# Optimization experiments

Measured on AMD Instinct MI355X. Metric: run time of the kernel, lower is better.

Reference implementation:

```python
import jax, jax.numpy as jnp
import numpy as np

B, C, H, W = 4, 64, 128, 128
K = 9  # 3x3 kernel taps
OFFSET_SCALE = 1.0
EPS = 1e-5


def conv2d(x, w, b):
    # x: [B,Cin,H,W], w: [Cout,Cin,3,3] -> [B,Cout,H,W] (SAME padding, stride 1)
    out = jax.lax.conv_general_dilated(x, w, (1, 1), 'SAME',
                                       dimension_numbers=('NCHW', 'OIHW', 'NCHW'))
    return out + b[None, :, None, None]


def deform_conv(x, w, b, ow, ob):
    # DCN-style 3x3 deformable conv, stride 1, pad 1, 1 deformable group.
    Bn, Cin, Hh, Ww = x.shape
    off = conv2d(x, ow, ob).reshape(Bn, K, 2, Hh, Ww) * OFFSET_SCALE  # (dy,dx) per tap
    dy = jnp.array([-1, -1, -1, 0, 0, 0, 1, 1, 1], jnp.float32)
    dx = jnp.array([-1, 0, 1, -1, 0, 1, -1, 0, 1], jnp.float32)
    iy = jnp.arange(Hh, dtype=jnp.float32)
    ix = jnp.arange(Ww, dtype=jnp.float32)
    # sampling coords: [B,K,H,W]
    cy = iy[None, None, :, None] + dy[None, :, None, None] + off[:, :, 0]
    cx = ix[None, None, None, :] + dx[None, :, None, None] + off[:, :, 1]
    y0 = jnp.floor(cy); x0 = jnp.floor(cx)
    wy = cy - y0;       wx = cx - x0
    y0i = y0.astype(jnp.int32); x0i = x0.astype(jnp.int32)
    vals = x.reshape(Bn, Cin, Hh * Ww)

    def gather(yi, xi, wgt):
        valid = ((yi >= 0) & (yi < Hh) & (xi >= 0) & (xi < Ww)).astype(x.dtype)
        idx = (jnp.clip(yi, 0, Hh - 1) * Ww + jnp.clip(xi, 0, Ww - 1)).reshape(Bn, 1, K * Hh * Ww)
        g = jnp.take_along_axis(vals, idx, axis=2).reshape(Bn, Cin, K, Hh, Ww)
        return g * (wgt * valid)[:, None]  # zero padding outside image

    samp = (gather(y0i,     x0i,     (1 - wy) * (1 - wx))
          + gather(y0i,     x0i + 1, (1 - wy) * wx)
          + gather(y0i + 1, x0i,     wy * (1 - wx))
          + gather(y0i + 1, x0i + 1, wy * wx))  # [B,Cin,K,H,W]
    out = jnp.einsum('bckhw,ock->bohw', samp, w.reshape(w.shape[0], Cin, K))
    return out + b[None, :, None, None]


def group_norm1(x, gamma, beta):
    # num_groups=1: normalize over (C,H,W) per sample
    m = jnp.mean(x, axis=(1, 2, 3), keepdims=True)
    v = jnp.var(x, axis=(1, 2, 3), keepdims=True)
    return (x - m) * jax.lax.rsqrt(v + EPS) * gamma[None, :, None, None] + beta[None, :, None, None]


def setup_inputs() -> dict:
    key = jax.random.key(0)
    ks = jax.random.split(key, 6)
    n = lambda k, shape, s: jax.random.normal(k, shape, dtype=jnp.float32) * s
    return {
        'x':   jax.random.normal(ks[0], (B, C, H, W), dtype=jnp.float32),
        'w1':  n(ks[1], (C, C, 3, 3), 0.05), 'b1': jnp.zeros((C,), jnp.float32),
        'ow1': n(ks[2], (2 * K, C, 3, 3), 0.01), 'ob1': jnp.zeros((2 * K,), jnp.float32),
        'g1':  jnp.ones((C,), jnp.float32), 'be1': jnp.zeros((C,), jnp.float32),
        'w2':  n(ks[3], (C, C, 3, 3), 0.05), 'b2': jnp.zeros((C,), jnp.float32),
        'ow2': n(ks[4], (2 * K, C, 3, 3), 0.01), 'ob2': jnp.zeros((2 * K,), jnp.float32),
        'g2':  jnp.ones((C,), jnp.float32), 'be2': jnp.zeros((C,), jnp.float32),
    }


def reference(x, w1, b1, ow1, ob1, g1, be1, w2, b2, ow2, ob2, g2, be2):
    # block1: deform_conv -> GN(1) -> relu -> (dropout=identity), + identity shortcut
    h = jax.nn.relu(group_norm1(deform_conv(x, w1, b1, ow1, ob1), g1, be1)) + x
    # block2: same, residual on h
    h = jax.nn.relu(group_norm1(deform_conv(h, w2, b2, ow2, ob2), g2, be2)) + h
    return h
```

## Files before the change

kernel.cpp:

```cpp
#include <hip/hip_runtime.h>
#include <hip/hip_bf16.h>
#include <math.h>

constexpr int Bz = 4, Cc = 64, Hh = 128, Ww = 128, Kk = 9;
constexpr int HW = Hh * Ww;
constexpr float EPSf = 1e-5f;
constexpr int CK = Cc * Kk;

typedef __attribute__((ext_vector_type(8))) short short8;
typedef __attribute__((ext_vector_type(4))) float f32x4;

__device__ __forceinline__ ushort f32_to_bf16(float f) {
    uint u = __float_as_uint(f);
    return (ushort)((u + 0x7fffu + ((u >> 16) & 1u)) >> 16);
}

__global__ void frag_kernel(const float* __restrict__ w1, const float* __restrict__ w2,
                            const float* __restrict__ ow1, const float* __restrict__ ow2,
                            ushort* __restrict__ wA1, ushort* __restrict__ wA2,
                            ushort* __restrict__ oA1, ushort* __restrict__ oA2) {
    int tid = blockIdx.x * 256 + threadIdx.x;
    if (tid >= 110592) return;
    const float* src; ushort* dst; int e; int cout;
    if (tid < 36864)        { src = w1;  dst = wA1; e = tid;         cout = 64; }
    else if (tid < 73728)   { src = w2;  dst = wA2; e = tid - 36864; cout = 64; }
    else if (tid < 92160)   { src = ow1; dst = oA1; e = tid - 73728; cout = 18; }
    else                    { src = ow2; dst = oA2; e = tid - 92160; cout = 18; }
    int j = e & 7, l = (e >> 3) & 63, kk = (e >> 9) % 18, wo = e / 9216;
    int oc = wo * 16 + (l & 15);
    int kidx = kk * 32 + ((l >> 4) * 8) + j;
    int tap = kidx >> 6, c = kidx & 63;
    dst[e] = (oc < cout) ? f32_to_bf16(src[oc * CK + c * 9 + tap]) : (ushort)0;
}

__global__ __launch_bounds__(256)
void nhwc_kernel(const float* __restrict__ src, ushort* __restrict__ dst) {
    __shared__ float s_t[64][65];
    int blk = blockIdx.x;
    int p0 = (blk & 255) * 64;
    int b = blk >> 8;
    int t = threadIdx.x;
    int tp = t & 63;
    #pragma unroll
    for (int i = 0; i < 16; i++) {
        int c = i * 4 + (t >> 6);
        s_t[c][tp] = src[((size_t)(b * 64 + c)) * HW + p0 + tp];
    }
    __syncthreads();
    #pragma unroll
    for (int i = 0; i < 16; i++) {
        int pl = i * 4 + (t >> 6);
        dst[((size_t)b * HW + p0 + pl) * 64 + tp] = f32_to_bf16(s_t[tp][pl]);
    }
}

__global__ __launch_bounds__(512, 6)
void deform_fused_kernel(const ushort* __restrict__ xnh, const ushort* __restrict__ wA,
                         const ushort* __restrict__ owA, const float* __restrict__ bias,
                         const float* __restrict__ obias, float* __restrict__ y,
                         float* __restrict__ part) {
    __shared__ __align__(16) ushort s_a[32 * 584];
    __shared__ __align__(16) uint   s_aw[32 * 9 * 8];
    float (*off_s2)[32][18] = reinterpret_cast<float (*)[32][18]>(s_a);

    int blk = blockIdx.x;
    int wt = blk & 3;
    int h  = (blk >> 2) & 127;
    int b  = blk >> 9;
    int w0 = wt * 32;
    int t = threadIdx.x;
    int wv = t >> 6, lane = t & 63;
    const ushort* xnb = xnh + (size_t)b * HW * 64;

    {
        int wo = wv & 1, ph = (wv >> 1) & 1, kh = wv >> 2;
        int g = lane >> 4, li = lane & 15;
        int px = ph * 16 + li;
        f32x4 oacc;
        #pragma unroll
        for (int r = 0; r < 4; r++) {
            int oc = wo * 16 + g * 4 + r;
            oacc[r] = (kh == 0 && oc < 18) ? obias[oc] : 0.f;
        }
        const short8* owp = reinterpret_cast<const short8*>(owA) + (wo * 18) * 64 + lane;
        #pragma unroll
        for (int kki = 0; kki < 9; kki++) {
            int kk = kh * 9 + kki;
            int tap = kk >> 1;
            int ky = tap / 3 - 1, kx = tap - (tap / 3) * 3 - 1;
            int c0 = (kk & 1) * 32 + g * 8;
            int gy = h + ky, gx = w0 + px + kx;
            bool valid = ((unsigned)gy < 128u) && ((unsigned)gx < 128u);
            short8 bf = {0, 0, 0, 0, 0, 0, 0, 0};
            if (valid)
                bf = *reinterpret_cast<const short8*>(&xnb[(((gy << 7) + gx) << 6) + c0]);
            short8 af = owp[kk * 64];
            oacc = __builtin_amdgcn_mfma_f32_16x16x32_bf16(af, bf, oacc, 0, 0, 0);
        }
        #pragma unroll
        for (int r = 0; r < 4; r++) {
            int oc = wo * 16 + g * 4 + r;
            if (oc < 18) off_s2[kh][px][oc] = oacc[r];
        }
    }
    __syncthreads();

    uint aw_l[8];
    bool has_unit = (t < 288);
    if (has_unit) {
        int px = t / 9, k = t - px * 9;
        int ky = k / 3 - 1, kx = k - (k / 3) * 3 - 1;
        float ody = off_s2[0][px][2 * k]     + off_s2[1][px][2 * k];
        float odx = off_s2[0][px][2 * k + 1] + off_s2[1][px][2 * k + 1];
        float cy = (float)(h + ky) + ody;
        float cx = (float)(w0 + px + kx) + odx;
        float fy = floorf(cy), fx = floorf(cx);
        float wy = cy - fy, wx = cx - fx;
        int y0 = (int)fy, x0 = (int)fx;
        int yy[2] = {y0, y0 + 1}; int xx[2] = {x0, x0 + 1};
        float wyv[2] = {1.f - wy, wy}; float wxv[2] = {1.f - wx, wx};
        #pragma unroll
        for (int ci = 0; ci < 2; ci++)
        #pragma unroll
        for (int cj = 0; cj < 2; cj++) {
            int yv = yy[ci], xv = xx[cj];
            bool val = ((unsigned)yv < 128u) && ((unsigned)xv < 128u);
            int ycl = min(max(yv, 0), 127), xcl = min(max(xv, 0), 127);
            int slot = ci * 2 + cj;
            aw_l[slot * 2]     = (uint)(((ycl << 7) + xcl) << 7);
            aw_l[slot * 2 + 1] = __float_as_uint(val ? wyv[ci] * wxv[cj] : 0.f);
        }
    }
    __syncthreads();
    if (has_unit) {
        uint base = (uint)t * 8;
        #pragma unroll
        for (int i = 0; i < 8; i++) s_aw[base + i] = aw_l[i];
    }
    __syncthreads();

    {
        int sub = lane >> 3;
        int ci  = lane & 7;
        int co  = ci << 4;
        const char* xnc = reinterpret_cast<const char*>(xnb);
        char* s_ab = reinterpret_cast<char*>(s_a);
        #pragma unroll
        for (int i = 0; i < 5; i++) {
            int lu = i * 8 + sub;
            if (lu < 36) {
                int U = wv * 36 + lu;
                int px = U / 9;
                int tap = U - px * 9;
                const uint4 q0 = *reinterpret_cast<const uint4*>(&s_aw[U * 8]);
                const uint4 q1 = *reinterpret_cast<const uint4*>(&s_aw[U * 8 + 4]);
                uint4 v00 = *reinterpret_cast<const uint4*>(xnc + (q0.x + co));
                uint4 v01 = *reinterpret_cast<const uint4*>(xnc + (q0.z + co));
                uint4 v10 = *reinterpret_cast<const uint4*>(xnc + (q1.x + co));
                uint4 v11 = *reinterpret_cast<const uint4*>(xnc + (q1.z + co));
                float w00 = __uint_as_float(q0.y), w01 = __uint_as_float(q0.w);
                float w10 = __uint_as_float(q1.y), w11 = __uint_as_float(q1.w);
                float a0, a1, a2, a3, a4, a5, a6, a7;
                #define LO(u) __uint_as_float((u) << 16)
                #define HI(u) __uint_as_float((u) & 0xffff0000u)
                a0 = w00 * LO(v00.x); a1 = w00 * HI(v00.x);
                a2 = w00 * LO(v00.y); a3 = w00 * HI(v00.y);
                a4 = w00 * LO(v00.z); a5 = w00 * HI(v00.z);
                a6 = w00 * LO(v00.w); a7 = w00 * HI(v00.w);
                a0 = fmaf(w01, LO(v01.x), a0); a1 = fmaf(w01, HI(v01.x), a1);
                a2 = fmaf(w01, LO(v01.y), a2); a3 = fmaf(w01, HI(v01.y), a3);
                a4 = fmaf(w01, LO(v01.z), a4); a5 = fmaf(w01, HI(v01.z), a5);
                a6 = fmaf(w01, LO(v01.w), a6); a7 = fmaf(w01, HI(v01.w), a7);
                a0 = fmaf(w10, LO(v10.x), a0); a1 = fmaf(w10, HI(v10.x), a1);
                a2 = fmaf(w10, LO(v10.y), a2); a3 = fmaf(w10, HI(v10.y), a3);
                a4 = fmaf(w10, LO(v10.z), a4); a5 = fmaf(w10, HI(v10.z), a5);
                a6 = fmaf(w10, LO(v10.w), a6); a7 = fmaf(w10, HI(v10.w), a7);
                a0 = fmaf(w11, LO(v11.x), a0); a1 = fmaf(w11, HI(v11.x), a1);
                a2 = fmaf(w11, LO(v11.y), a2); a3 = fmaf(w11, HI(v11.y), a3);
                a4 = fmaf(w11, LO(v11.z), a4); a5 = fmaf(w11, HI(v11.z), a5);
                a6 = fmaf(w11, LO(v11.w), a6); a7 = fmaf(w11, HI(v11.w), a7);
                #undef LO
                #undef HI
                float2 p01; p01.x = a0; p01.y = a1;
                float2 p23; p23.x = a2; p23.y = a3;
                float2 p45; p45.x = a4; p45.y = a5;
                float2 p67; p67.x = a6; p67.y = a7;
                __hip_bfloat162 b01 = __float22bfloat162_rn(p01);
                __hip_bfloat162 b23 = __float22bfloat162_rn(p23);
                __hip_bfloat162 b45 = __float22bfloat162_rn(p45);
                __hip_bfloat162 b67 = __float22bfloat162_rn(p67);
                uint4 outv;
                outv.x = *reinterpret_cast<uint*>(&b01);
                outv.y = *reinterpret_cast<uint*>(&b23);
                outv.z = *reinterpret_cast<uint*>(&b45);
                outv.w = *reinterpret_cast<uint*>(&b67);
                *reinterpret_cast<uint4*>(s_ab + px * 1168 + tap * 128 + co) = outv;
            }
        }
    }
    __syncthreads();

    int wo = wv & 3, ph = wv >> 2;
    int g = lane >> 4, li = lane & 15;
    f32x4 acc;
    const float* bp = bias + wo * 16 + g * 4;
    acc.x = bp[0]; acc.y = bp[1]; acc.z = bp[2]; acc.w = bp[3];
    const short8* ap = reinterpret_cast<const short8*>(wA) + (wo * 18) * 64 + lane;
    const ushort* sp = s_a + (ph * 16 + li) * 584 + g * 8;
    #pragma unroll
    for (int kk = 0; kk < 18; kk++) {
        short8 af = ap[kk * 64];
        short8 bf = *reinterpret_cast<const short8*>(sp + kk * 32);
        acc = __builtin_amdgcn_mfma_f32_16x16x32_bf16(af, bf, acc, 0, 0, 0);
    }
    size_t ybase = ((size_t)(b * 64 + wo * 16 + g * 4)) * HW + h * Ww + w0 + ph * 16 + li;
    y[ybase]           = acc.x;
    y[ybase + HW]      = acc.y;
    y[ybase + 2 * HW]  = acc.z;
    y[ybase + 3 * HW]  = acc.w;

    float s  = acc.x + acc.y + acc.z + acc.w;
    float s2 = acc.x * acc.x + acc.y * acc.y + acc.z * acc.z + acc.w * acc.w;
    #pragma unroll
    for (int o = 32; o > 0; o >>= 1) {
        s  += __shfl_down(s, o);
        s2 += __shfl_down(s2, o);
    }
    float* redbuf = reinterpret_cast<float*>(s_aw);
    if (lane == 0) { redbuf[wv * 2] = s; redbuf[wv * 2 + 1] = s2; }
    __syncthreads();
    if (t == 0) {
        float a = 0.f, c2 = 0.f;
        #pragma unroll
        for (int i = 0; i < 8; i++) { a += redbuf[i * 2]; c2 += redbuf[i * 2 + 1]; }
        part[blk * 2]     = a;
        part[blk * 2 + 1] = c2;
    }
}

__device__ __forceinline__ void gn_reduce_stats(const float* __restrict__ part, int b,
                                                int t, float& m_out, float& rs_out) {
    __shared__ float ls[4][2];
    __shared__ float s_ms[2];
    int i0 = (b * 512 + t) * 2, i1 = (b * 512 + 256 + t) * 2;
    float s  = part[i0]     + part[i1];
    float s2 = part[i0 + 1] + part[i1 + 1];
    #pragma unroll
    for (int o = 32; o > 0; o >>= 1) {
        s  += __shfl_down(s, o);
        s2 += __shfl_down(s2, o);
    }
    int wave = t >> 6, lane = t & 63;
    if (lane == 0) { ls[wave][0] = s; ls[wave][1] = s2; }
    __syncthreads();
    if (t == 0) {
        float a = 0.f, c = 0.f;
        #pragma unroll
        for (int i = 0; i < 4; i++) { a += ls[i][0]; c += ls[i][1]; }
        const float n = (float)(Cc * HW);
        float m = a / n;
        float var = c / n - m * m;
        s_ms[0] = m;
        s_ms[1] = rsqrtf(var + EPSf);
    }
    __syncthreads();
    m_out = s_ms[0];
    rs_out = s_ms[1];
}

__global__ __launch_bounds__(256)
void gn_fin1_kernel(const float* __restrict__ y, const float* __restrict__ res,
                    const float* __restrict__ g, const float* __restrict__ be,
                    const float* __restrict__ part, float* __restrict__ h1,
                    ushort* __restrict__ hnh) {
    __shared__ float s_t[64][65];
    int blk = blockIdx.x;
    int p0 = (blk & 255) * 64;
    int b = blk >> 8;
    int t = threadIdx.x;
    int tp = t & 63;
    float m, rs;
    gn_reduce_stats(part, b, t, m, rs);
    #pragma unroll
    for (int i = 0; i < 16; i++) {
        int c = i * 4 + (t >> 6);
        size_t idx = ((size_t)(b * 64 + c)) * HW + p0 + tp;
        float v = (y[idx] - m) * rs * g[c] + be[c];
        v = fmaxf(v, 0.f) + res[idx];
        h1[idx] = v;
        s_t[c][tp] = v;
    }
    __syncthreads();
    #pragma unroll
    for (int i = 0; i < 16; i++) {
        int pl = i * 4 + (t >> 6);
        hnh[((size_t)b * HW + p0 + pl) * 64 + tp] = f32_to_bf16(s_t[tp][pl]);
    }
}

__global__ __launch_bounds__(256)
void gn_fin2_kernel(const float* __restrict__ y, const float* __restrict__ res,
                    const float* __restrict__ g, const float* __restrict__ be,
                    const float* __restrict__ part, float* __restrict__ out) {
    int idx = (blockIdx.x * 256 + threadIdx.x) * 4;
    int c = (idx >> 14) & 63;
    int b = idx >> 20;
    float m, rs;
    gn_reduce_stats(part, b, threadIdx.x, m, rs);
    float gc = g[c], bc = be[c];
    float4 yv = *reinterpret_cast<const float4*>(y + idx);
    float4 rv = *reinterpret_cast<const float4*>(res + idx);
    float4 o;
    o.x = fmaxf((yv.x - m) * rs * gc + bc, 0.f) + rv.x;
    o.y = fmaxf((yv.y - m) * rs * gc + bc, 0.f) + rv.y;
    o.z = fmaxf((yv.z - m) * rs * gc + bc, 0.f) + rv.z;
    o.w = fmaxf((yv.w - m) * rs * gc + bc, 0.f) + rv.w;
    *reinterpret_cast<float4*>(out + idx) = o;
}

extern "C" void kernel_launch(void* const* d_in, const int* in_sizes, int n_in,
                              void* d_out, int out_size, void* d_ws, size_t ws_size,
                              hipStream_t stream) {
    const float* x   = (const float*)d_in[0];
    const float* w1  = (const float*)d_in[1];
    const float* b1  = (const float*)d_in[2];
    const float* ow1 = (const float*)d_in[3];
    const float* ob1 = (const float*)d_in[4];
    const float* g1  = (const float*)d_in[5];
    const float* be1 = (const float*)d_in[6];
    const float* w2  = (const float*)d_in[7];
    const float* b2  = (const float*)d_in[8];
    const float* ow2 = (const float*)d_in[9];
    const float* ob2 = (const float*)d_in[10];
    const float* g2  = (const float*)d_in[11];
    const float* be2 = (const float*)d_in[12];
    float* out = (float*)d_out;

    float* ws    = (float*)d_ws;
    float* ybuf  = ws;
    float* h1    = ybuf + (size_t)Bz * Cc * HW;
    ushort* xnh  = (ushort*)(h1 + (size_t)Bz * Cc * HW);
    ushort* hnh  = xnh + (size_t)Bz * HW * 64;
    ushort* wA1  = hnh + (size_t)Bz * HW * 64;
    ushort* wA2  = wA1 + 36864;
    ushort* owA1 = wA2 + 36864;
    ushort* owA2 = owA1 + 18432;
    float* part  = (float*)(owA2 + 18432);

    frag_kernel<<<(110592 + 255) / 256, 256, 0, stream>>>(w1, w2, ow1, ow2, wA1, wA2, owA1, owA2);
    nhwc_kernel<<<Bz * (HW / 64), 256, 0, stream>>>(x, xnh);

    deform_fused_kernel<<<Bz * Hh * (Ww / 32), 512, 0, stream>>>(xnh, wA1, owA1, b1, ob1, ybuf, part);
    gn_fin1_kernel<<<Bz * (HW / 64), 256, 0, stream>>>(ybuf, x, g1, be1, part, h1, hnh);

    deform_fused_kernel<<<Bz * Hh * (Ww / 32), 512, 0, stream>>>(hnh, wA2, owA2, b2, ob2, ybuf, part);
    gn_fin2_kernel<<<Bz * Cc * HW / 1024, 256, 0, stream>>>(ybuf, h1, g2, be2, part, out);
}
```

Measured before the change: 122.6 us.

## Halve deform conv tile to 16 pixels and compute bilinear corners in gather

Shrinks the fused deformable-conv block from 32 pixels/512 threads to 16 pixels/256 threads, which doubles the grid and halves LDS per block, with the aim of raising occupancy and improving load balance. The per-sample corner table (8 words per unit) is replaced by a packed y0/x0 word plus the fractional weights. Each gather lane now recomputes the four clamped addresses and validity-masked weights itself, removing one barrier and the LDS staging. The GN stats reduction is updated to sum 1024 partials per sample. The cost is some redundant integer and float work per lane, plus reloading the weight fragments for each smaller tile.

```diff
diff --git a/kernel.cpp b/kernel.cpp
--- a/kernel.cpp
+++ b/kernel.cpp
@@ -54,28 +54,29 @@
     }
 }
 
-__global__ __launch_bounds__(512, 6)
+__global__ __launch_bounds__(256, 8)
 void deform_fused_kernel(const ushort* __restrict__ xnh, const ushort* __restrict__ wA,
                          const ushort* __restrict__ owA, const float* __restrict__ bias,
                          const float* __restrict__ obias, float* __restrict__ y,
                          float* __restrict__ part) {
-    __shared__ __align__(16) ushort s_a[32 * 584];
-    __shared__ __align__(16) uint   s_aw[32 * 9 * 8];
-    float (*off_s2)[32][18] = reinterpret_cast<float (*)[32][18]>(s_a);
+    __shared__ __align__(16) ushort s_a[16 * 584];
+    __shared__ uint   s_yx[144];
+    __shared__ float2 s_wyx[144];
+    float (*off_s2)[16][18] = reinterpret_cast<float (*)[16][18]>(s_a);
 
     int blk = blockIdx.x;
-    int wt = blk & 3;
-    int h  = (blk >> 2) & 127;
-    int b  = blk >> 9;
-    int w0 = wt * 32;
+    int wt = blk & 7;
+    int h  = (blk >> 3) & 127;
+    int b  = blk >> 10;
+    int w0 = wt * 16;
     int t = threadIdx.x;
     int wv = t >> 6, lane = t & 63;
     const ushort* xnb = xnh + (size_t)b * HW * 64;
 
     {
-        int wo = wv & 1, ph = (wv >> 1) & 1, kh = wv >> 2;
+        int wo = wv & 1, kh = wv >> 1;
         int g = lane >> 4, li = lane & 15;
-        int px = ph * 16 + li;
+        int px = li;
         f32x4 oacc;
         #pragma unroll
         for (int r = 0; r < 4; r++) {
@@ -105,9 +106,7 @@
     }
     __syncthreads();
 
-    uint aw_l[8];
-    bool has_unit = (t < 288);
-    if (has_unit) {
+    if (t < 144) {
         int px = t / 9, k = t - px * 9;
         int ky = k / 3 - 1, kx = k - (k / 3) * 3 - 1;
         float ody = off_s2[0][px][2 * k]     + off_s2[1][px][2 * k];
@@ -115,27 +114,10 @@
         float cy = (float)(h + ky) + ody;
         float cx = (float)(w0 + px + kx) + odx;
         float fy = floorf(cy), fx = floorf(cx);
-        float wy = cy - fy, wx = cx - fx;
         int y0 = (int)fy, x0 = (int)fx;
-        int yy[2] = {y0, y0 + 1}; int xx[2] = {x0, x0 + 1};
-        float wyv[2] = {1.f - wy, wy}; float wxv[2] = {1.f - wx, wx};
-        #pragma unroll
-        for (int ci = 0; ci < 2; ci++)
-        #pragma unroll
-        for (int cj = 0; cj < 2; cj++) {
-            int yv = yy[ci], xv = xx[cj];
-            bool val = ((unsigned)yv < 128u) && ((unsigned)xv < 128u);
-            int ycl = min(max(yv, 0), 127), xcl = min(max(xv, 0), 127);
-            int slot = ci * 2 + cj;
-            aw_l[slot * 2]     = (uint)(((ycl << 7) + xcl) << 7);
-            aw_l[slot * 2 + 1] = __float_as_uint(val ? wyv[ci] * wxv[cj] : 0.f);
-        }
-    }
-    __syncthreads();
-    if (has_unit) {
-        uint base = (uint)t * 8;
-        #pragma unroll
-        for (int i = 0; i < 8; i++) s_aw[base + i] = aw_l[i];
+        s_yx[t] = (uint)(y0 & 0xffff) | ((uint)x0 << 16);
+        float2 wv2; wv2.x = cy - fy; wv2.y = cx - fx;
+        s_wyx[t] = wv2;
     }
     __syncthreads();
 
@@ -152,14 +134,28 @@
                 int U = wv * 36 + lu;
                 int px = U / 9;
                 int tap = U - px * 9;
-                const uint4 q0 = *reinterpret_cast<const uint4*>(&s_aw[U * 8]);
-                const uint4 q1 = *reinterpret_cast<const uint4*>(&s_aw[U * 8 + 4]);
-                uint4 v00 = *reinterpret_cast<const uint4*>(xnc + (q0.x + co));
-                uint4 v01 = *reinterpret_cast<const uint4*>(xnc + (q0.z + co));
-                uint4 v10 = *reinterpret_cast<const uint4*>(xnc + (q1.x + co));
-                uint4 v11 = *reinterpret_cast<const uint4*>(xnc + (q1.z + co));
-                float w00 = __uint_as_float(q0.y), w01 = __uint_as_float(q0.w);
-                float w10 = __uint_as_float(q1.y), w11 = __uint_as_float(q1.w);
+                uint yx = s_yx[U];
+                float2 wv2 = s_wyx[U];
+                int y0 = (short)(yx & 0xffffu);
+                int x0 = (short)(yx >> 16);
+                float wy = wv2.x, wx = wv2.y;
+                int y1 = y0 + 1, x1 = x0 + 1;
+                bool vy0 = (unsigned)y0 < 128u, vy1 = (unsigned)y1 < 128u;
+                bool vx0 = (unsigned)x0 < 128u, vx1 = (unsigned)x1 < 128u;
+                int yc0 = min(max(y0, 0), 127), yc1 = min(max(y1, 0), 127);
+                int xc0 = min(max(x0, 0), 127), xc1 = min(max(x1, 0), 127);
+                uint a00 = (uint)(((yc0 << 7) + xc0) << 7) + co;
+                uint a01 = (uint)(((yc0 << 7) + xc1) << 7) + co;
+                uint a10 = (uint)(((yc1 << 7) + xc0) << 7) + co;
+                uint a11 = (uint)(((yc1 << 7) + xc1) << 7) + co;
+                float w00 = (vy0 && vx0) ? (1.f - wy) * (1.f - wx) : 0.f;
+                float w01 = (vy0 && vx1) ? (1.f - wy) * wx : 0.f;
+                float w10 = (vy1 && vx0) ? wy * (1.f - wx) : 0.f;
+                float w11 = (vy1 && vx1) ? wy * wx : 0.f;
+                uint4 v00 = *reinterpret_cast<const uint4*>(xnc + a00);
+                uint4 v01 = *reinterpret_cast<const uint4*>(xnc + a01);
+                uint4 v10 = *reinterpret_cast<const uint4*>(xnc + a10);
+                uint4 v11 = *reinterpret_cast<const uint4*>(xnc + a11);
                 float a0, a1, a2, a3, a4, a5, a6, a7;
                 #define LO(u) __uint_as_float((u) << 16)
                 #define HI(u) __uint_as_float((u) & 0xffff0000u)
@@ -200,20 +196,20 @@
     }
     __syncthreads();
 
-    int wo = wv & 3, ph = wv >> 2;
+    int wo = wv;
     int g = lane >> 4, li = lane & 15;
     f32x4 acc;
     const float* bp = bias + wo * 16 + g * 4;
     acc.x = bp[0]; acc.y = bp[1]; acc.z = bp[2]; acc.w = bp[3];
     const short8* ap = reinterpret_cast<const short8*>(wA) + (wo * 18) * 64 + lane;
-    const ushort* sp = s_a + (ph * 16 + li) * 584 + g * 8;
+    const ushort* sp = s_a + li * 584 + g * 8;
     #pragma unroll
     for (int kk = 0; kk < 18; kk++) {
         short8 af = ap[kk * 64];
         short8 bf = *reinterpret_cast<const short8*>(sp + kk * 32);
         acc = __builtin_amdgcn_mfma_f32_16x16x32_bf16(af, bf, acc, 0, 0, 0);
     }
-    size_t ybase = ((size_t)(b * 64 + wo * 16 + g * 4)) * HW + h * Ww + w0 + ph * 16 + li;
+    size_t ybase = ((size_t)(b * 64 + wo * 16 + g * 4)) * HW + h * Ww + w0 + li;
     y[ybase]           = acc.x;
     y[ybase + HW]      = acc.y;
     y[ybase + 2 * HW]  = acc.z;
@@ -226,13 +222,13 @@
         s  += __shfl_down(s, o);
         s2 += __shfl_down(s2, o);
     }
-    float* redbuf = reinterpret_cast<float*>(s_aw);
+    float* redbuf = reinterpret_cast<float*>(s_yx);
     if (lane == 0) { redbuf[wv * 2] = s; redbuf[wv * 2 + 1] = s2; }
     __syncthreads();
     if (t == 0) {
         float a = 0.f, c2 = 0.f;
         #pragma unroll
-        for (int i = 0; i < 8; i++) { a += redbuf[i * 2]; c2 += redbuf[i * 2 + 1]; }
+        for (int i = 0; i < 4; i++) { a += redbuf[i * 2]; c2 += redbuf[i * 2 + 1]; }
         part[blk * 2]     = a;
         part[blk * 2 + 1] = c2;
     }
@@ -242,9 +238,11 @@
                                                 int t, float& m_out, float& rs_out) {
     __shared__ float ls[4][2];
     __shared__ float s_ms[2];
-    int i0 = (b * 512 + t) * 2, i1 = (b * 512 + 256 + t) * 2;
-    float s  = part[i0]     + part[i1];
-    float s2 = part[i0 + 1] + part[i1 + 1];
+    int base = b * 1024 + t;
+    float s  = part[base * 2]            + part[(base + 256) * 2]
+             + part[(base + 512) * 2]    + part[(base + 768) * 2];
+    float s2 = part[base * 2 + 1]        + part[(base + 256) * 2 + 1]
+             + part[(base + 512) * 2 + 1] + part[(base + 768) * 2 + 1];
     #pragma unroll
     for (int o = 32; o > 0; o >>= 1) {
         s  += __shfl_down(s, o);
@@ -350,9 +348,9 @@
     frag_kernel<<<(110592 + 255) / 256, 256, 0, stream>>>(w1, w2, ow1, ow2, wA1, wA2, owA1, owA2);
     nhwc_kernel<<<Bz * (HW / 64), 256, 0, stream>>>(x, xnh);
 
-    deform_fused_kernel<<<Bz * Hh * (Ww / 32), 512, 0, stream>>>(xnh, wA1, owA1, b1, ob1, ybuf, part);
+    deform_fused_kernel<<<Bz * Hh * (Ww / 16), 256, 0, stream>>>(xnh, wA1, owA1, b1, ob1, ybuf, part);
     gn_fin1_kernel<<<Bz * (HW / 64), 256, 0, stream>>>(ybuf, x, g1, be1, part, h1, hnh);
 
-    deform_fused_kernel<<<Bz * Hh * (Ww / 32), 512, 0, stream>>>(hnh, wA2, owA2, b2, ob2, ybuf, part);
+    deform_fused_kernel<<<Bz * Hh * (Ww / 16), 256, 0, stream>>>(hnh, wA2, owA2, b2, ob2, ybuf, part);
     gn_fin2_kernel<<<Bz * Cc * HW / 1024, 256, 0, stream>>>(ybuf, h1, g2, be2, part, out);
 }
```

Measured after the change: 124.3 us. About the same (+1.4%).

## Stage input halo tile in LDS for offset conv and bilinear gathers

Applied to the files above, without the earlier changes.

Each block now loads a 5x36-pixel, 64-channel bf16 halo tile of the input into shared memory once. Both the offset-conv MFMA operand loads and the bilinear sampling gathers read from it, falling back to global memory, flagged by a high address bit, when a sample lands outside the tile. This is meant to cut repeated global/L2 gather traffic, since the offsets are small and most samples stay near the pixel. It costs about 26KB more LDS, a block-wide sync, and a divergent branch per unit. The occupancy hint in launch_bounds is removed, so fewer blocks may fit per CU.

```diff
diff --git a/kernel.cpp b/kernel.cpp
--- a/kernel.cpp
+++ b/kernel.cpp
@@ -6,6 +6,8 @@
 constexpr int HW = Hh * Ww;
 constexpr float EPSf = 1e-5f;
 constexpr int CK = Cc * Kk;
+
+constexpr int TROWS = 5, TCOLS = 36, TPITCH = 144;
 
 typedef __attribute__((ext_vector_type(8))) short short8;
 typedef __attribute__((ext_vector_type(4))) float f32x4;
@@ -54,11 +56,12 @@
     }
 }
 
-__global__ __launch_bounds__(512, 6)
+__global__ __launch_bounds__(512)
 void deform_fused_kernel(const ushort* __restrict__ xnh, const ushort* __restrict__ wA,
                          const ushort* __restrict__ owA, const float* __restrict__ bias,
                          const float* __restrict__ obias, float* __restrict__ y,
                          float* __restrict__ part) {
+    __shared__ __align__(16) char   s_x[TROWS * TCOLS * TPITCH];
     __shared__ __align__(16) ushort s_a[32 * 584];
     __shared__ __align__(16) uint   s_aw[32 * 9 * 8];
     float (*off_s2)[32][18] = reinterpret_cast<float (*)[32][18]>(s_a);
@@ -71,6 +74,22 @@
     int t = threadIdx.x;
     int wv = t >> 6, lane = t & 63;
     const ushort* xnb = xnh + (size_t)b * HW * 64;
+    const char* xnc = reinterpret_cast<const char*>(xnb);
+
+    #pragma unroll
+    for (int r = 0; r < 3; r++) {
+        int e = r * 512 + t;
+        if (e < TROWS * TCOLS * 8) {
+            int ch = e & 7, px = e >> 3;
+            int row = px / TCOLS, col = px - row * TCOLS;
+            int gy = h - 2 + row, gx = w0 - 2 + col;
+            uint4 v = {0u, 0u, 0u, 0u};
+            if ((unsigned)gy < 128u && (unsigned)gx < 128u)
+                v = *reinterpret_cast<const uint4*>(xnc + ((((gy << 7) + gx) << 7) + ch * 16));
+            *reinterpret_cast<uint4*>(&s_x[px * TPITCH + ch * 16]) = v;
+        }
+    }
+    __syncthreads();
 
     {
         int wo = wv & 1, ph = (wv >> 1) & 1, kh = wv >> 2;
@@ -88,12 +107,9 @@
             int kk = kh * 9 + kki;
             int tap = kk >> 1;
             int ky = tap / 3 - 1, kx = tap - (tap / 3) * 3 - 1;
-            int c0 = (kk & 1) * 32 + g * 8;
-            int gy = h + ky, gx = w0 + px + kx;
-            bool valid = ((unsigned)gy < 128u) && ((unsigned)gx < 128u);
-            short8 bf = {0, 0, 0, 0, 0, 0, 0, 0};
-            if (valid)
-                bf = *reinterpret_cast<const short8*>(&xnb[(((gy << 7) + gx) << 6) + c0]);
+            int cb = (kk & 1) * 64 + g * 16;
+            short8 bf = *reinterpret_cast<const short8*>(
+                &s_x[((ky + 2) * TCOLS + px + kx + 2) * TPITCH + cb]);
             short8 af = owp[kk * 64];
             oacc = __builtin_amdgcn_mfma_f32_16x16x32_bf16(af, bf, oacc, 0, 0, 0);
         }
@@ -117,19 +133,31 @@
         float fy = floorf(cy), fx = floorf(cx);
         float wy = cy - fy, wx = cx - fx;
         int y0 = (int)fy, x0 = (int)fx;
-        int yy[2] = {y0, y0 + 1}; int xx[2] = {x0, x0 + 1};
-        float wyv[2] = {1.f - wy, wy}; float wxv[2] = {1.f - wx, wx};
-        #pragma unroll
-        for (int ci = 0; ci < 2; ci++)
-        #pragma unroll
-        for (int cj = 0; cj < 2; cj++) {
-            int yv = yy[ci], xv = xx[cj];
-            bool val = ((unsigned)yv < 128u) && ((unsigned)xv < 128u);
-            int ycl = min(max(yv, 0), 127), xcl = min(max(xv, 0), 127);
-            int slot = ci * 2 + cj;
-            aw_l[slot * 2]     = (uint)(((ycl << 7) + xcl) << 7);
-            aw_l[slot * 2 + 1] = __float_as_uint(val ? wyv[ci] * wxv[cj] : 0.f);
-        }
+        int y1 = y0 + 1, x1 = x0 + 1;
+        bool vy0 = (unsigned)y0 < 128u, vy1 = (unsigned)y1 < 128u;
+        bool vx0 = (unsigned)x0 < 128u, vx1 = (unsigned)x1 < 128u;
+        int yc0 = min(max(y0, 0), 127), yc1 = min(max(y1, 0), 127);
+        int xc0 = min(max(x0, 0), 127), xc1 = min(max(x1, 0), 127);
+        int r0 = yc0 - (h - 2),  r1 = yc1 - (h - 2);
+        int c0t = xc0 - (w0 - 2), c1t = xc1 - (w0 - 2);
+        bool intile = ((unsigned)r0 < (unsigned)TROWS) && ((unsigned)r1 < (unsigned)TROWS)
+                   && ((unsigned)c0t < (unsigned)TCOLS) && ((unsigned)c1t < (unsigned)TCOLS);
+        uint a00, a01, a10, a11;
+        if (intile) {
+            a00 = (uint)((r0 * TCOLS + c0t) * TPITCH);
+            a01 = (uint)((r0 * TCOLS + c1t) * TPITCH);
+            a10 = (uint)((r1 * TCOLS + c0t) * TPITCH);
+            a11 = (uint)((r1 * TCOLS + c1t) * TPITCH);
+        } else {
+            a00 = (uint)(((yc0 << 7) + xc0) << 7) | 0x80000000u;
+            a01 = (uint)(((yc0 << 7) + xc1) << 7) | 0x80000000u;
+            a10 = (uint)(((yc1 << 7) + xc0) << 7) | 0x80000000u;
+            a11 = (uint)(((yc1 << 7) + xc1) << 7) | 0x80000000u;
+        }
+        aw_l[0] = a00; aw_l[1] = __float_as_uint((vy0 && vx0) ? (1.f - wy) * (1.f - wx) : 0.f);
+        aw_l[2] = a01; aw_l[3] = __float_as_uint((vy0 && vx1) ? (1.f - wy) * wx : 0.f);
+        aw_l[4] = a10; aw_l[5] = __float_as_uint((vy1 && vx0) ? wy * (1.f - wx) : 0.f);
+        aw_l[6] = a11; aw_l[7] = __float_as_uint((vy1 && vx1) ? wy * wx : 0.f);
     }
     __syncthreads();
     if (has_unit) {
@@ -143,7 +171,6 @@
         int sub = lane >> 3;
         int ci  = lane & 7;
         int co  = ci << 4;
-        const char* xnc = reinterpret_cast<const char*>(xnb);
         char* s_ab = reinterpret_cast<char*>(s_a);
         #pragma unroll
         for (int i = 0; i < 5; i++) {
@@ -152,12 +179,20 @@
                 int U = wv * 36 + lu;
                 int px = U / 9;
                 int tap = U - px * 9;
-                const uint4 q0 = *reinterpret_cast<const uint4*>(&s_aw[U * 8]);
-                const uint4 q1 = *reinterpret_cast<const uint4*>(&s_aw[U * 8 + 4]);
-                uint4 v00 = *reinterpret_cast<const uint4*>(xnc + (q0.x + co));
-                uint4 v01 = *reinterpret_cast<const uint4*>(xnc + (q0.z + co));
-                uint4 v10 = *reinterpret_cast<const uint4*>(xnc + (q1.x + co));
-                uint4 v11 = *reinterpret_cast<const uint4*>(xnc + (q1.z + co));
+                uint4 q0 = *reinterpret_cast<const uint4*>(&s_aw[U * 8]);
+                uint4 q1 = *reinterpret_cast<const uint4*>(&s_aw[U * 8 + 4]);
+                uint4 v00, v01, v10, v11;
+                if (!(q0.x & 0x80000000u)) {
+                    v00 = *reinterpret_cast<const uint4*>(&s_x[q0.x + co]);
+                    v01 = *reinterpret_cast<const uint4*>(&s_x[q0.z + co]);
+                    v10 = *reinterpret_cast<const uint4*>(&s_x[q1.x + co]);
+                    v11 = *reinterpret_cast<const uint4*>(&s_x[q1.z + co]);
+                } else {
+                    v00 = *reinterpret_cast<const uint4*>(xnc + ((q0.x & 0x7fffffffu) + co));
+                    v01 = *reinterpret_cast<const uint4*>(xnc + ((q0.z & 0x7fffffffu) + co));
+                    v10 = *reinterpret_cast<const uint4*>(xnc + ((q1.x & 0x7fffffffu) + co));
+                    v11 = *reinterpret_cast<const uint4*>(xnc + ((q1.z & 0x7fffffffu) + co));
+                }
                 float w00 = __uint_as_float(q0.y), w01 = __uint_as_float(q0.w);
                 float w10 = __uint_as_float(q1.y), w11 = __uint_as_float(q1.w);
                 float a0, a1, a2, a3, a4, a5, a6, a7;
```

Result: no change. 121.1 us (-1.2%).
